# Optimization experiments

Measured on AMD Instinct MI355X. Metric: run time of the kernel, lower is better.

The kernel has to match this reference:

```python
import jax, jax.numpy as jnp
import numpy as np

NUM_GROUPS = 32
EPS = 1e-5


def group_norm(x, scale, bias):
    # x: [b, c, h, w]
    b, c, h, w = x.shape
    xg = x.reshape(b, NUM_GROUPS, c // NUM_GROUPS, h, w)
    mean = jnp.mean(xg, axis=(2, 3, 4), keepdims=True)
    var = jnp.var(xg, axis=(2, 3, 4), keepdims=True)
    xg = (xg - mean) * jax.lax.rsqrt(var + EPS)
    xn = xg.reshape(b, c, h, w)
    return xn * scale[None, :, None, None] + bias[None, :, None, None]


def conv1x1(x, w, b):
    # x: [b, c_in, h, w], w: [c_out, c_in], b: [c_out]
    return jnp.einsum('bchw,dc->bdhw', x, w) + b[None, :, None, None]


def setup_inputs() -> dict:
    key = jax.random.key(0)
    ks = jax.random.split(key, 11)
    B, C, H, W = 16, 512, 32, 32
    s = 1.0 / np.sqrt(C)
    inp = {
        'x': jax.random.normal(ks[0], (B, C, H, W), jnp.float32),
        'gn_scale': jnp.ones((C,), jnp.float32),
        'gn_bias': jnp.zeros((C,), jnp.float32),
        'wq': jax.random.normal(ks[1], (C, C), jnp.float32) * s,
        'bq': jnp.zeros((C,), jnp.float32),
        'wk': jax.random.normal(ks[2], (C, C), jnp.float32) * s,
        'bk': jnp.zeros((C,), jnp.float32),
        'wv': jax.random.normal(ks[3], (C, C), jnp.float32) * s,
        'bv': jnp.zeros((C,), jnp.float32),
        'wp': jax.random.normal(ks[4], (C, C), jnp.float32) * s,
        'bp': jnp.zeros((C,), jnp.float32),
    }
    return inp


def reference(x, gn_scale, gn_bias, wq, bq, wk, bk, wv, bv, wp, bp):
    b, c, h, w = x.shape
    xn = group_norm(x, gn_scale, gn_bias)
    q = conv1x1(xn, wq, bq).reshape(b, c, h * w)  # [b, c, n]
    k = conv1x1(xn, wk, bk).reshape(b, c, h * w)
    v = conv1x1(xn, wv, bv).reshape(b, c, h * w)
    # attn[b, i, j] = sum_c q[b, c, i] * k[b, c, j]
    attn = jnp.einsum('bci,bcj->bij', q, k) * (c ** -0.5)
    A = jax.nn.softmax(attn, axis=-1)
    # out[b, c, i] = sum_j A[b, i, j] * v[b, c, j]
    out = jnp.einsum('bij,bcj->bci', A, v).reshape(b, c, h, w)
    scores = conv1x1(out, wp, bp)
    return x + scores
```

## Files before the change

kernel.cpp:

```cpp
#include <hip/hip_runtime.h>

typedef __bf16 bf16x8 __attribute__((ext_vector_type(8)));
typedef float  f32x4  __attribute__((ext_vector_type(4)));

__device__ __forceinline__ unsigned short f2bf(float f) {
    union { float f; unsigned int u; } x; x.f = f;
    unsigned int r = (x.u + 0x7FFFu + ((x.u >> 16) & 1u)) >> 16;
    return (unsigned short)r;
}

typedef const __attribute__((address_space(1))) unsigned short gu16;
typedef __attribute__((address_space(3)))       unsigned short lu16;
__device__ __forceinline__ void gl_lds16(const unsigned short* g, unsigned short* l) {
    __builtin_amdgcn_global_load_lds((gu16*)g, (lu16*)l, 16, 0, 0);
}

__device__ __forceinline__ void stage8(
    const unsigned short* __restrict__ Ab, int lda,
    const unsigned short* __restrict__ Bb, int ldb,
    unsigned short* LB, int s, int s_max, int wave, int lane)
{
    if (s >= s_max) return;
    const int tau  = s >> 2;
    const int pi   = s & 3;
    const int isA  = pi >> 1;
    const int half = pi & 1;
    unsigned short* dst = LB + (isA ? 0 : 32768) + (tau & 1) * 16384 + half * 8192 + wave * 512;
    const unsigned short* src = isA ? Ab : Bb;
    const int ld = isA ? lda : ldb;
    const int R  = half * 128 + wave * 8 + (lane >> 3);
    const int kc = tau * 64 + (((lane & 7) ^ ((lane >> 5) << 1)) << 3);
    gl_lds16(src + (long)R * ld + kc,        dst);
    gl_lds16(src + (long)(R + 64) * ld + kc, dst + 4096);
}

template<int NT>
__device__ __forceinline__ void gemm8_core(
    const unsigned short* __restrict__ Ab, int lda,
    const unsigned short* __restrict__ Bb, int ldb,
    f32x4 (&acc)[8][4], unsigned short* LB)
{
    const int tid  = threadIdx.x;
    const int lane = tid & 63;
    const int wave = tid >> 6;
    const int wM   = wave >> 2;
    const int wN   = wave & 3;
    const int l16  = lane & 15;
    const int quad = lane >> 4;
    const int ckx  = quad ^ (((l16 >> 2) & 1) << 1);
    const int aoff = wM * 8192 + l16 * 64 + ckx * 8;
    const int boff = 32768 + (wN >> 1) * 8192 + ((wN & 1) * 64 + l16) * 64 + ckx * 8;

    #pragma unroll
    for (int s = 0; s < 7; ++s)
        stage8(Ab, lda, Bb, ldb, LB, s, 4 * NT, wave, lane);
    asm volatile("s_waitcnt vmcnt(6)" ::: "memory");
    __builtin_amdgcn_s_barrier();
    __builtin_amdgcn_sched_barrier(0);

    bf16x8 af[4][2], bf[4][2];

#define RD_A(buf, mh)                                                         \
    _Pragma("unroll")                                                         \
    for (int m = 0; m < 4; ++m)                                               \
        _Pragma("unroll")                                                     \
        for (int kk = 0; kk < 2; ++kk)                                        \
            af[m][kk] = *(const bf16x8*)&LB[(buf) * 16384 + aoff + ((mh) * 4 + m) * 1024 + kk * 32];
#define RD_B(buf)                                                             \
    _Pragma("unroll")                                                         \
    for (int n = 0; n < 4; ++n)                                               \
        _Pragma("unroll")                                                     \
        for (int kk = 0; kk < 2; ++kk)                                        \
            bf[n][kk] = *(const bf16x8*)&LB[(buf) * 16384 + boff + n * 1024 + kk * 32];
#define MF(mh, nh)                                                            \
    __builtin_amdgcn_s_setprio(1);                                            \
    _Pragma("unroll")                                                         \
    for (int m = 0; m < 4; ++m)                                               \
        _Pragma("unroll")                                                     \
        for (int n = 0; n < 2; ++n)                                           \
            _Pragma("unroll")                                                 \
            for (int kk = 0; kk < 2; ++kk)                                    \
                acc[(mh)*4+m][(nh)*2+n] = __builtin_amdgcn_mfma_f32_16x16x32_bf16( \
                    af[m][kk], bf[(nh)*2+n][kk], acc[(mh)*4+m][(nh)*2+n], 0, 0, 0); \
    __builtin_amdgcn_s_setprio(0);
#define BARS do { __builtin_amdgcn_s_barrier(); __builtin_amdgcn_sched_barrier(0); } while (0)
#define LGW  do { asm volatile("s_waitcnt lgkmcnt(0)" ::: "memory"); __builtin_amdgcn_sched_barrier(0); } while (0)

    const int NITER = NT / 2;
    for (int i = 0; i < NITER; ++i) {
        const int s0 = 6 + 8 * i;
        RD_B(0) RD_A(0, 0)
        stage8(Ab, lda, Bb, ldb, LB, s0 + 1, 4 * NT, wave, lane);
        BARS; LGW;
        MF(0, 0)
        BARS;
        stage8(Ab, lda, Bb, ldb, LB, s0 + 2, 4 * NT, wave, lane);
        BARS;
        MF(0, 1)
        BARS;
        RD_A(0, 1)
        stage8(Ab, lda, Bb, ldb, LB, s0 + 3, 4 * NT, wave, lane);
        BARS; LGW;
        MF(1, 0)
        BARS;
        stage8(Ab, lda, Bb, ldb, LB, s0 + 4, 4 * NT, wave, lane);
        BARS;
        MF(1, 1)
        if (i == NITER - 1) { asm volatile("s_waitcnt vmcnt(0)" ::: "memory"); }
        else                { asm volatile("s_waitcnt vmcnt(6)" ::: "memory"); }
        BARS;
        RD_B(1) RD_A(1, 0)
        stage8(Ab, lda, Bb, ldb, LB, s0 + 5, 4 * NT, wave, lane);
        BARS; LGW;
        MF(0, 0)
        BARS;
        stage8(Ab, lda, Bb, ldb, LB, s0 + 6, 4 * NT, wave, lane);
        BARS;
        MF(0, 1)
        BARS;
        RD_A(1, 1)
        stage8(Ab, lda, Bb, ldb, LB, s0 + 7, 4 * NT, wave, lane);
        BARS; LGW;
        MF(1, 0)
        BARS;
        stage8(Ab, lda, Bb, ldb, LB, s0 + 8, 4 * NT, wave, lane);
        BARS;
        MF(1, 1)
        if (i < NITER - 1) { asm volatile("s_waitcnt vmcnt(6)" ::: "memory"); }
        BARS;
    }
#undef RD_A
#undef RD_B
#undef MF
#undef BARS
#undef LGW
}

__global__ __launch_bounds__(512, 2) void p8_k(
    const unsigned short* __restrict__ qT,
    const unsigned short* __restrict__ kT,
    unsigned short* __restrict__ Sb,
    float* __restrict__ lsum,
    float alpha)
{
    __shared__ __align__(16) unsigned short LB[65536];
    const int z = blockIdx.z;
    const unsigned short* Ab = qT + (long)z * 524288 + (long)(blockIdx.y * 256) * 512;
    const unsigned short* Bb = kT + (long)z * 524288 + (long)(blockIdx.x * 256) * 512;
    f32x4 acc[8][4] = {};
    gemm8_core<8>(Ab, 512, Bb, 512, acc, LB);

    const int lane = threadIdx.x & 63, wave = threadIdx.x >> 6;
    const int wM = wave >> 2, wN = wave & 3;
    const int l16 = lane & 15, quad = lane >> 4;
    const int gm0 = blockIdx.y * 256 + wM * 128;
    const int gn0 = blockIdx.x * 256 + wN * 64;
    unsigned short* scr = LB + wave * 8192;

    float rs[8][4];
    #pragma unroll
    for (int mi = 0; mi < 8; ++mi) { rs[mi][0] = rs[mi][1] = rs[mi][2] = rs[mi][3] = 0.f; }
    #pragma unroll
    for (int mi = 0; mi < 8; ++mi)
        #pragma unroll
        for (int ni = 0; ni < 4; ++ni) {
            f32x4 v = acc[mi][ni];
            #pragma unroll
            for (int r = 0; r < 4; ++r) {
                float e = __expf(v[r] * alpha);
                rs[mi][r] += e;
                const int row = mi * 16 + quad * 4 + r;
                const int col = ni * 16 + l16;
                scr[row * 64 + (((col >> 3) ^ (row & 7)) << 3) + (col & 7)] = f2bf(e);
            }
        }
    #pragma unroll
    for (int mi = 0; mi < 8; ++mi)
        #pragma unroll
        for (int r = 0; r < 4; ++r) {
            float s = rs[mi][r];
            s += __shfl_xor(s, 1); s += __shfl_xor(s, 2);
            s += __shfl_xor(s, 4); s += __shfl_xor(s, 8);
            if (l16 == 0)
                atomicAdd(&lsum[(long)z * 1024 + gm0 + mi * 16 + quad * 4 + r], s);
        }
    unsigned short* dst = Sb + (long)z * 1048576;
    #pragma unroll
    for (int it = 0; it < 16; ++it) {
        const int row = it * 8 + (lane >> 3);
        const int ck  = lane & 7;
        uint4 vv = *(uint4*)&scr[row * 64 + ((ck ^ (row & 7)) << 3)];
        *(uint4*)&dst[(long)(gm0 + row) * 1024 + gn0 + ck * 8] = vv;
    }
}

__global__ __launch_bounds__(512, 2) void qkv8_k(
    const unsigned short* __restrict__ Wqkv,
    const unsigned short* __restrict__ xnT,
    unsigned short* __restrict__ qT,
    unsigned short* __restrict__ kT,
    unsigned short* __restrict__ vB,
    const float* __restrict__ bqkv)
{
    __shared__ __align__(16) unsigned short LB[65536];
    const int z = blockIdx.z;
    const unsigned short* Ab = Wqkv + (long)(blockIdx.y * 256) * 512;
    const unsigned short* Bb = xnT + (long)z * 524288 + (long)(blockIdx.x * 256) * 512;
    f32x4 acc[8][4] = {};
    gemm8_core<8>(Ab, 512, Bb, 512, acc, LB);

    const int lane = threadIdx.x & 63, wave = threadIdx.x >> 6;
    const int wM = wave >> 2, wN = wave & 3;
    const int l16 = lane & 15, quad = lane >> 4;
    const int gm0 = blockIdx.y * 256 + wM * 128;
    const int gn0 = blockIdx.x * 256 + wN * 64;
    const int mat = blockIdx.y >> 1;
    const int ml0 = gm0 & 511;
    const long zb = (long)z * 524288;
    unsigned short* scr = LB + wave * 8192;

    if (mat == 2) {
        #pragma unroll
        for (int mi = 0; mi < 8; ++mi)
            #pragma unroll
            for (int ni = 0; ni < 4; ++ni) {
                f32x4 v = acc[mi][ni];
                #pragma unroll
                for (int r = 0; r < 4; ++r) {
                    const int row = mi * 16 + quad * 4 + r;
                    const int col = ni * 16 + l16;
                    scr[row * 64 + (((col >> 3) ^ (row & 7)) << 3) + (col & 7)] =
                        f2bf(v[r] + bqkv[gm0 + row]);
                }
            }
        #pragma unroll
        for (int it = 0; it < 16; ++it) {
            const int row = it * 8 + (lane >> 3);
            const int ck  = lane & 7;
            uint4 vv = *(uint4*)&scr[row * 64 + ((ck ^ (row & 7)) << 3)];
            *(uint4*)&vB[zb + (long)(ml0 + row) * 1024 + gn0 + ck * 8] = vv;
        }
    } else {
        unsigned short* dstm = (mat == 0) ? qT : kT;
        #pragma unroll
        for (int mi = 0; mi < 8; ++mi)
            #pragma unroll
            for (int ni = 0; ni < 4; ++ni) {
                f32x4 v = acc[mi][ni];
                const int nl = ni * 16 + l16;
                const int ch = mi * 2 + (quad >> 1);
                const int m4 = gm0 + mi * 16 + quad * 4;
                ushort4 p;
                p.x = f2bf(v[0] + bqkv[m4 + 0]);
                p.y = f2bf(v[1] + bqkv[m4 + 1]);
                p.z = f2bf(v[2] + bqkv[m4 + 2]);
                p.w = f2bf(v[3] + bqkv[m4 + 3]);
                *(ushort4*)&scr[nl * 128 + ((ch ^ (nl & 15)) << 3) + (quad & 1) * 4] = p;
            }
        #pragma unroll
        for (int it = 0; it < 16; ++it) {
            const int nl  = it * 4 + (lane >> 4);
            const int chl = lane & 15;
            uint4 vv = *(uint4*)&scr[nl * 128 + ((chl ^ (nl & 15)) << 3)];
            *(uint4*)&dstm[zb + (long)(gn0 + nl) * 512 + ml0 + chl * 8] = vv;
        }
    }
}

__device__ __forceinline__ void stage_tiles(
    const unsigned short* __restrict__ Ab, int lda,
    const unsigned short* __restrict__ Bb, int ldb,
    int k0, unsigned short* Ad, unsigned short* Bd,
    int wave, int r0, int c0)
{
    gl_lds16(Ab + (long)r0 * lda + c0 + k0,        Ad + wave * 512);
    gl_lds16(Ab + (long)(r0 + 64) * lda + c0 + k0, Ad + 2048 + wave * 512);
    gl_lds16(Bb + (long)r0 * ldb + c0 + k0,        Bd + wave * 512);
    gl_lds16(Bb + (long)(r0 + 64) * ldb + c0 + k0, Bd + 2048 + wave * 512);
}

__device__ __forceinline__ void gemm_core_db(
    const unsigned short* __restrict__ Ab, int lda,
    const unsigned short* __restrict__ Bb, int ldb,
    int K, f32x4 (&acc)[4][4],
    unsigned short* As, unsigned short* Bs)
{
    const int tid  = threadIdx.x;
    const int lane = tid & 63;
    const int wave = tid >> 6;
    const int wm   = (wave >> 1) * 64;
    const int wn   = (wave & 1) * 64;
    const int l16  = lane & 15;
    const int quad = lane >> 4;

    const int r0 = wave * 16 + (lane >> 2);
    const int c0 = ((lane & 3) ^ ((lane >> 3) & 3)) * 8;

    stage_tiles(Ab, lda, Bb, ldb, 0, As, Bs, wave, r0, c0);

    const int sw8 = ((l16 >> 1) & 3) * 8;

    int sel = 0;
    for (int k0 = 0; k0 < K; k0 += 32) {
        __syncthreads();
        if (k0 + 32 < K)
            stage_tiles(Ab, lda, Bb, ldb, k0 + 32,
                        As + (sel ^ 1) * 4096, Bs + (sel ^ 1) * 4096, wave, r0, c0);

        const unsigned short* Ap = As + sel * 4096;
        const unsigned short* Bp = Bs + sel * 4096;
        bf16x8 af[4], bfr[4];
        #pragma unroll
        for (int mi = 0; mi < 4; mi++)
            af[mi] = *(const bf16x8*)&Ap[(wm + mi * 16 + l16) * 32 + ((quad * 8) ^ sw8)];
        #pragma unroll
        for (int ni = 0; ni < 4; ni++)
            bfr[ni] = *(const bf16x8*)&Bp[(wn + ni * 16 + l16) * 32 + ((quad * 8) ^ sw8)];
        #pragma unroll
        for (int mi = 0; mi < 4; mi++)
            #pragma unroll
            for (int ni = 0; ni < 4; ni++)
                acc[mi][ni] = __builtin_amdgcn_mfma_f32_16x16x32_bf16(af[mi], bfr[ni], acc[mi][ni], 0, 0, 0);
        sel ^= 1;
    }
}

template<typename OutT, bool TRANS_OUT, bool HAS_BIAS, bool HAS_RESID,
         bool EXP_SUM, bool ROW_SCALE>
__global__ __launch_bounds__(256) void gemm_k(
    const unsigned short* __restrict__ Ag, long sA, int lda,
    const unsigned short* __restrict__ Bg, long sB, int ldb,
    OutT* __restrict__ Cg, long sC, int ldc,
    const float* __restrict__ bias,
    const float* __restrict__ resid, long sR,
    float* __restrict__ lsum, long sL,
    float alpha, int K)
{
    __shared__ __align__(16) unsigned short LB[16384];
    unsigned short* As = LB;
    unsigned short* Bs = LB + 8192;

    const unsigned short* Ab = Ag + (long)blockIdx.z * sA + (long)(blockIdx.y * 128) * lda;
    const unsigned short* Bb = Bg + (long)blockIdx.z * sB + (long)(blockIdx.x * 128) * ldb;

    f32x4 acc[4][4] = {};
    gemm_core_db(Ab, lda, Bb, ldb, K, acc, As, Bs);

    const int lane = threadIdx.x & 63;
    const int wave = threadIdx.x >> 6;
    const int l16  = lane & 15;
    const int quad = lane >> 4;
    const int mb = blockIdx.y * 128 + (wave >> 1) * 64;
    const int nb = blockIdx.x * 128 + (wave & 1) * 64;

    if constexpr (sizeof(OutT) == 2) {
        __syncthreads();
        unsigned short* scr = LB + wave * 4096;

        #pragma unroll
        for (int mi = 0; mi < 4; mi++) {
            float rsum[4];
            if constexpr (EXP_SUM) { rsum[0] = rsum[1] = rsum[2] = rsum[3] = 0.f; }
            #pragma unroll
            for (int ni = 0; ni < 4; ni++) {
                f32x4 v = acc[mi][ni];
                float invl;
                if constexpr (ROW_SCALE) invl = 1.f / lsum[(long)blockIdx.z * sL + nb + ni * 16 + l16];
                float o[4];
                #pragma unroll
                for (int r = 0; r < 4; r++) {
                    float val = v[r] * alpha;
                    if constexpr (HAS_BIAS) val += bias[mb + mi * 16 + quad * 4 + r];
                    if constexpr (EXP_SUM) { val = __expf(val); rsum[r] += val; }
                    if constexpr (ROW_SCALE) val *= invl;
                    o[r] = val;
                }
                if constexpr (TRANS_OUT) {
                    const int nl = ni * 16 + l16;
                    const int ch = mi * 2 + (quad >> 1);
                    ushort4 p; p.x = f2bf(o[0]); p.y = f2bf(o[1]); p.z = f2bf(o[2]); p.w = f2bf(o[3]);
                    *(ushort4*)&scr[nl * 64 + ((ch ^ (nl & 7)) * 8) + (quad & 1) * 4] = p;
                } else {
                    #pragma unroll
                    for (int r = 0; r < 4; r++) {
                        const int ml = mi * 16 + quad * 4 + r;
                        const int nc = ni * 2 + (l16 >> 3);
                        scr[ml * 64 + ((nc ^ (ml & 7)) * 8) + (l16 & 7)] = f2bf(o[r]);
                    }
                }
            }
            if constexpr (EXP_SUM) {
                const int m0 = mb + mi * 16 + quad * 4;
                #pragma unroll
                for (int r = 0; r < 4; r++) {
                    float s = rsum[r];
                    s += __shfl_xor(s, 1); s += __shfl_xor(s, 2);
                    s += __shfl_xor(s, 4); s += __shfl_xor(s, 8);
                    if (l16 == 0)
                        atomicAdd(&lsum[(long)blockIdx.z * sL + m0 + r], s);
                }
            }
        }
        __syncthreads();

        const int ch2 = lane & 7;
        const int rr  = lane >> 3;
        unsigned short* Cs = (unsigned short*)Cg + (long)blockIdx.z * sC;
        if constexpr (TRANS_OUT) {
            unsigned short* dst = Cs + mb + ch2 * 8;
            #pragma unroll
            for (int it = 0; it < 8; it++) {
                const int nl = rr + it * 8;
                uint4 v = *(uint4*)&scr[nl * 64 + ((ch2 ^ (nl & 7)) * 8)];
                *(uint4*)(dst + (long)(nb + nl) * ldc) = v;
            }
        } else {
            unsigned short* dst = Cs + nb + ch2 * 8;
            #pragma unroll
            for (int it = 0; it < 8; it++) {
                const int ml = rr + it * 8;
                uint4 v = *(uint4*)&scr[ml * 64 + ((ch2 ^ (ml & 7)) * 8)];
                *(uint4*)(dst + (long)(mb + ml) * ldc) = v;
            }
        }
    } else {
        #pragma unroll
        for (int mi = 0; mi < 4; mi++) {
            #pragma unroll
            for (int ni = 0; ni < 4; ni++) {
                f32x4 v = acc[mi][ni];
                const int m0 = mb + mi * 16 + quad * 4;
                const int n  = nb + ni * 16 + l16;
                const long base = (long)blockIdx.z * sC;
                #pragma unroll
                for (int r = 0; r < 4; r++) {
                    float val = v[r] * alpha;
                    if (HAS_BIAS) val += bias[m0 + r];
                    if (HAS_RESID) val += resid[(long)blockIdx.z * sR + (long)(m0 + r) * ldc + n];
                    ((float*)Cg)[base + (long)(m0 + r) * ldc + n] = val;
                }
            }
        }
    }
}

__global__ __launch_bounds__(256) void gn_k(
    const float* __restrict__ x, const float* __restrict__ gsc,
    const float* __restrict__ gbi, unsigned short* __restrict__ xnT)
{
    __shared__ __align__(16) unsigned short ln[16 * 1024];
    __shared__ float red[8];
    const int b = blockIdx.y, g = blockIdx.x;
    const int tid = threadIdx.x, lane = tid & 63, wv = tid >> 6;

    const float4* x4 = (const float4*)(x + ((long)b * 512 + g * 16) * 1024);
    float4 vals[16];
    float s = 0.f, ss = 0.f;
    #pragma unroll
    for (int i = 0; i < 16; i++) {
        float4 v = x4[tid + i * 256];
        vals[i] = v;
        s  += v.x + v.y + v.z + v.w;
        ss += v.x * v.x + v.y * v.y + v.z * v.z + v.w * v.w;
    }
    for (int o = 32; o; o >>= 1) { s += __shfl_down(s, o); ss += __shfl_down(ss, o); }
    if (lane == 0) { red[wv * 2] = s; red[wv * 2 + 1] = ss; }
    __syncthreads();
    const float S  = red[0] + red[2] + red[4] + red[6];
    const float SS = red[1] + red[3] + red[5] + red[7];
    const float mean = S * (1.f / 16384.f);
    const float var  = SS * (1.f / 16384.f) - mean * mean;
    const float inv  = rsqrtf(var + 1e-5f);

    #pragma unroll
    for (int i = 0; i < 16; i++) {
        const int idx = tid + i * 256;
        const int c   = idx >> 8;
        const float sc = gsc[g * 16 + c] * inv;
        const float bi = gbi[g * 16 + c] - mean * sc;
        float4 v = vals[i];
        ushort4 p;
        p.x = f2bf(v.x * sc + bi); p.y = f2bf(v.y * sc + bi);
        p.z = f2bf(v.z * sc + bi); p.w = f2bf(v.w * sc + bi);
        ((ushort4*)ln)[idx] = p;
    }
    __syncthreads();

    unsigned short* op = xnT + (long)b * 1024 * 512 + g * 16;
    for (int rep = 0; rep < 4; rep++) {
        const int n = rep * 256 + tid;
        union { unsigned short u[16]; uint4 v[2]; } t;
        #pragma unroll
        for (int c = 0; c < 16; c++) t.u[c] = ln[c * 1024 + n];
        *(uint4*)&op[(long)n * 512]     = t.v[0];
        *(uint4*)&op[(long)n * 512 + 8] = t.v[1];
    }
}

__global__ __launch_bounds__(256) void wconv_k(
    const float* __restrict__ w0, const float* __restrict__ w1,
    const float* __restrict__ w2, const float* __restrict__ w3,
    const float* __restrict__ b0, const float* __restrict__ b1,
    const float* __restrict__ b2,
    unsigned short* __restrict__ out, float* __restrict__ bqkv,
    float* __restrict__ lsum)
{
    const int m = blockIdx.y;
    const int i = blockIdx.x * 256 + threadIdx.x;
    if (m == 4) {
        if (i < 384) {
            const int which = i >> 7, off = i & 127;
            const float* src = (which == 0) ? b0 : (which == 1) ? b1 : b2;
            ((float4*)bqkv)[i] = ((const float4*)src)[off];
        }
        if (i < 16384) lsum[i] = 0.f;
        return;
    }
    const float* src = (m == 0) ? w0 : (m == 1) ? w1 : (m == 2) ? w2 : w3;
    float4 v = ((const float4*)src)[i];
    ushort4 o; o.x = f2bf(v.x); o.y = f2bf(v.y); o.z = f2bf(v.z); o.w = f2bf(v.w);
    ((ushort4*)(out + (long)m * 262144))[i] = o;
}

extern "C" void kernel_launch(void* const* d_in, const int* in_sizes, int n_in,
                              void* d_out, int out_size, void* d_ws, size_t ws_size,
                              hipStream_t stream)
{
    const float* x   = (const float*)d_in[0];
    const float* gsc = (const float*)d_in[1];
    const float* gbi = (const float*)d_in[2];
    const float* wq  = (const float*)d_in[3];
    const float* bq  = (const float*)d_in[4];
    const float* wk  = (const float*)d_in[5];
    const float* bk  = (const float*)d_in[6];
    const float* wv  = (const float*)d_in[7];
    const float* bv  = (const float*)d_in[8];
    const float* wp  = (const float*)d_in[9];
    const float* bp  = (const float*)d_in[10];
    float* out = (float*)d_out;

    char* ws = (char*)d_ws;
    unsigned short* xnT = (unsigned short*)(ws);
    unsigned short* qT  = (unsigned short*)(ws + 16777216);
    unsigned short* kT  = (unsigned short*)(ws + 33554432);
    unsigned short* vB  = (unsigned short*)(ws + 50331648);
    unsigned short* Sb  = (unsigned short*)(ws + 67108864);
    unsigned short* Wb  = (unsigned short*)(ws + 100663296);
    float*          bqkv= (float*)        (ws + 102760448);
    float*          Lb  = (float*)        (ws + 102768640);
    unsigned short* OT  = xnT;

    const long sBCN = 512L * 1024;

    wconv_k<<<dim3(256, 5), 256, 0, stream>>>(wq, wk, wv, wp, bq, bk, bv, Wb, bqkv, Lb);
    gn_k<<<dim3(32, 16), 256, 0, stream>>>(x, gsc, gbi, xnT);

    qkv8_k<<<dim3(4, 6, 16), 512, 0, stream>>>(Wb, xnT, qT, kT, vB, bqkv);

    p8_k<<<dim3(4, 4, 16), 512, 0, stream>>>(qT, kT, Sb, Lb, 0.044194173824159216f);

    gemm_k<unsigned short, true, false, false, false, true>
        <<<dim3(8, 4, 16), 256, 0, stream>>>(
        vB, sBCN, 1024, Sb, 1048576L, 1024, OT, sBCN, 512,
        nullptr, nullptr, 0, Lb, 1024, 1.f, 1024);

    gemm_k<float, false, true, true, false, false>
        <<<dim3(8, 4, 16), 256, 0, stream>>>(
        Wb + 786432, 0, 512, OT, sBCN, 512, out, sBCN, 1024, bp, x, sBCN,
        nullptr, 0, 1.f, 512);
}
```

Before: 224.4 us.

## Generalize 8-wave pipelined GEMM core to 128-row tiles; use for QKV and AV

Templates the 8-wave global_load_lds pipelined GEMM core on the A-tile height so it can run with 128-row A tiles. The QKV projection moves to 128x256 tiles with twice as many blocks, and the attention-times-V GEMM moves from the 4-wave double-buffered kernel to this deeper pipeline. Weight conversion is merged into the group-norm launch to save one launch, and the generic gemm_k is specialised into a final projection kernel. The aim is better load balance across CUs and more latency hiding in the AV GEMM, with less B-tile reuse per block as the trade-off.

```diff
diff --git a/kernel.cpp b/kernel.cpp
--- a/kernel.cpp
+++ b/kernel.cpp
@@ -15,30 +15,35 @@
     __builtin_amdgcn_global_load_lds((gu16*)g, (lu16*)l, 16, 0, 0);
 }
 
-__device__ __forceinline__ void stage8(
+template<int NT, int BMH>
+__device__ __forceinline__ void stage8g(
     const unsigned short* __restrict__ Ab, int lda,
     const unsigned short* __restrict__ Bb, int ldb,
-    unsigned short* LB, int s, int s_max, int wave, int lane)
-{
-    if (s >= s_max) return;
+    unsigned short* LB, int s, int wave, int lane)
+{
+    if (s >= 4 * NT) return;
     const int tau  = s >> 2;
     const int pi   = s & 3;
-    const int isA  = pi >> 1;
     const int half = pi & 1;
-    unsigned short* dst = LB + (isA ? 0 : 32768) + (tau & 1) * 16384 + half * 8192 + wave * 512;
-    const unsigned short* src = isA ? Ab : Bb;
-    const int ld = isA ? lda : ldb;
-    const int R  = half * 128 + wave * 8 + (lane >> 3);
-    const int kc = tau * 64 + (((lane & 7) ^ ((lane >> 5) << 1)) << 3);
-    gl_lds16(src + (long)R * ld + kc,        dst);
-    gl_lds16(src + (long)(R + 64) * ld + kc, dst + 4096);
-}
-
-template<int NT>
+    const int kc   = tau * 64 + (((lane & 7) ^ ((lane >> 5) << 1)) << 3);
+    if (pi >= 2) {
+        unsigned short* dst = LB + (tau & 1) * (BMH * 8192) + half * (BMH * 4096) + wave * 512;
+        const int R = half * (BMH * 64) + wave * 8 + (lane >> 3);
+        gl_lds16(Ab + (long)R * lda + kc, dst);
+        if constexpr (BMH == 2) gl_lds16(Ab + (long)(R + 64) * lda + kc, dst + 4096);
+    } else {
+        unsigned short* dst = LB + (BMH * 16384) + (tau & 1) * 16384 + half * 8192 + wave * 512;
+        const int R = half * 128 + wave * 8 + (lane >> 3);
+        gl_lds16(Bb + (long)R * ldb + kc, dst);
+        gl_lds16(Bb + (long)(R + 64) * ldb + kc, dst + 4096);
+    }
+}
+
+template<int NT, int BMH>
 __device__ __forceinline__ void gemm8_core(
     const unsigned short* __restrict__ Ab, int lda,
     const unsigned short* __restrict__ Bb, int ldb,
-    f32x4 (&acc)[8][4], unsigned short* LB)
+    f32x4 (&acc)[4 * BMH][4], unsigned short* LB)
 {
     const int tid  = threadIdx.x;
     const int lane = tid & 63;
@@ -48,24 +53,27 @@
     const int l16  = lane & 15;
     const int quad = lane >> 4;
     const int ckx  = quad ^ (((l16 >> 2) & 1) << 1);
-    const int aoff = wM * 8192 + l16 * 64 + ckx * 8;
-    const int boff = 32768 + (wN >> 1) * 8192 + ((wN & 1) * 64 + l16) * 64 + ckx * 8;
+    const int aoff = wM * (BMH * 4096) + l16 * 64 + ckx * 8;
+    const int boff = BMH * 16384 + (wN >> 1) * 8192 + ((wN & 1) * 64 + l16) * 64 + ckx * 8;
+
+#define VMW do { if constexpr (BMH == 2) asm volatile("s_waitcnt vmcnt(6)" ::: "memory"); \
+                 else                    asm volatile("s_waitcnt vmcnt(5)" ::: "memory"); } while (0)
 
     #pragma unroll
     for (int s = 0; s < 7; ++s)
-        stage8(Ab, lda, Bb, ldb, LB, s, 4 * NT, wave, lane);
-    asm volatile("s_waitcnt vmcnt(6)" ::: "memory");
+        stage8g<NT, BMH>(Ab, lda, Bb, ldb, LB, s, wave, lane);
+    VMW;
     __builtin_amdgcn_s_barrier();
     __builtin_amdgcn_sched_barrier(0);
 
-    bf16x8 af[4][2], bf[4][2];
+    bf16x8 af[2 * BMH][2], bf[4][2];
 
 #define RD_A(buf, mh)                                                         \
     _Pragma("unroll")                                                         \
-    for (int m = 0; m < 4; ++m)                                               \
+    for (int m = 0; m < 2 * BMH; ++m)                                         \
         _Pragma("unroll")                                                     \
         for (int kk = 0; kk < 2; ++kk)                                        \
-            af[m][kk] = *(const bf16x8*)&LB[(buf) * 16384 + aoff + ((mh) * 4 + m) * 1024 + kk * 32];
+            af[m][kk] = *(const bf16x8*)&LB[(buf) * (BMH * 8192) + aoff + ((mh) * 2 * BMH + m) * 1024 + kk * 32];
 #define RD_B(buf)                                                             \
     _Pragma("unroll")                                                         \
     for (int n = 0; n < 4; ++n)                                               \
@@ -75,13 +83,13 @@
 #define MF(mh, nh)                                                            \
     __builtin_amdgcn_s_setprio(1);                                            \
     _Pragma("unroll")                                                         \
-    for (int m = 0; m < 4; ++m)                                               \
+    for (int m = 0; m < 2 * BMH; ++m)                                         \
         _Pragma("unroll")                                                     \
         for (int n = 0; n < 2; ++n)                                           \
             _Pragma("unroll")                                                 \
             for (int kk = 0; kk < 2; ++kk)                                    \
-                acc[(mh)*4+m][(nh)*2+n] = __builtin_amdgcn_mfma_f32_16x16x32_bf16( \
-                    af[m][kk], bf[(nh)*2+n][kk], acc[(mh)*4+m][(nh)*2+n], 0, 0, 0); \
+                acc[(mh) * 2 * BMH + m][(nh) * 2 + n] = __builtin_amdgcn_mfma_f32_16x16x32_bf16( \
+                    af[m][kk], bf[(nh) * 2 + n][kk], acc[(mh) * 2 * BMH + m][(nh) * 2 + n], 0, 0, 0); \
     __builtin_amdgcn_s_setprio(0);
 #define BARS do { __builtin_amdgcn_s_barrier(); __builtin_amdgcn_sched_barrier(0); } while (0)
 #define LGW  do { asm volatile("s_waitcnt lgkmcnt(0)" ::: "memory"); __builtin_amdgcn_sched_barrier(0); } while (0)
@@ -90,43 +98,43 @@
     for (int i = 0; i < NITER; ++i) {
         const int s0 = 6 + 8 * i;
         RD_B(0) RD_A(0, 0)
-        stage8(Ab, lda, Bb, ldb, LB, s0 + 1, 4 * NT, wave, lane);
+        stage8g<NT, BMH>(Ab, lda, Bb, ldb, LB, s0 + 1, wave, lane);
         BARS; LGW;
         MF(0, 0)
         BARS;
-        stage8(Ab, lda, Bb, ldb, LB, s0 + 2, 4 * NT, wave, lane);
+        stage8g<NT, BMH>(Ab, lda, Bb, ldb, LB, s0 + 2, wave, lane);
         BARS;
         MF(0, 1)
         BARS;
         RD_A(0, 1)
-        stage8(Ab, lda, Bb, ldb, LB, s0 + 3, 4 * NT, wave, lane);
+        stage8g<NT, BMH>(Ab, lda, Bb, ldb, LB, s0 + 3, wave, lane);
         BARS; LGW;
         MF(1, 0)
         BARS;
-        stage8(Ab, lda, Bb, ldb, LB, s0 + 4, 4 * NT, wave, lane);
+        stage8g<NT, BMH>(Ab, lda, Bb, ldb, LB, s0 + 4, wave, lane);
         BARS;
         MF(1, 1)
         if (i == NITER - 1) { asm volatile("s_waitcnt vmcnt(0)" ::: "memory"); }
-        else                { asm volatile("s_waitcnt vmcnt(6)" ::: "memory"); }
+        else                { VMW; }
         BARS;
         RD_B(1) RD_A(1, 0)
-        stage8(Ab, lda, Bb, ldb, LB, s0 + 5, 4 * NT, wave, lane);
+        stage8g<NT, BMH>(Ab, lda, Bb, ldb, LB, s0 + 5, wave, lane);
         BARS; LGW;
         MF(0, 0)
         BARS;
-        stage8(Ab, lda, Bb, ldb, LB, s0 + 6, 4 * NT, wave, lane);
+        stage8g<NT, BMH>(Ab, lda, Bb, ldb, LB, s0 + 6, wave, lane);
         BARS;
         MF(0, 1)
         BARS;
         RD_A(1, 1)
-        stage8(Ab, lda, Bb, ldb, LB, s0 + 7, 4 * NT, wave, lane);
+        stage8g<NT, BMH>(Ab, lda, Bb, ldb, LB, s0 + 7, wave, lane);
         BARS; LGW;
         MF(1, 0)
         BARS;
-        stage8(Ab, lda, Bb, ldb, LB, s0 + 8, 4 * NT, wave, lane);
+        stage8g<NT, BMH>(Ab, lda, Bb, ldb, LB, s0 + 8, wave, lane);
         BARS;
         MF(1, 1)
-        if (i < NITER - 1) { asm volatile("s_waitcnt vmcnt(6)" ::: "memory"); }
+        if (i < NITER - 1) { VMW; }
         BARS;
     }
 #undef RD_A
@@ -134,6 +142,7 @@
 #undef MF
 #undef BARS
 #undef LGW
+#undef VMW
 }
 
 __global__ __launch_bounds__(512, 2) void p8_k(
@@ -148,7 +157,7 @@
     const unsigned short* Ab = qT + (long)z * 524288 + (long)(blockIdx.y * 256) * 512;
     const unsigned short* Bb = kT + (long)z * 524288 + (long)(blockIdx.x * 256) * 512;
     f32x4 acc[8][4] = {};
-    gemm8_core<8>(Ab, 512, Bb, 512, acc, LB);
+    gemm8_core<8, 2>(Ab, 512, Bb, 512, acc, LB);
 
     const int lane = threadIdx.x & 63, wave = threadIdx.x >> 6;
     const int wM = wave >> 2, wN = wave & 3;
@@ -202,48 +211,48 @@
     unsigned short* __restrict__ vB,
     const float* __restrict__ bqkv)
 {
-    __shared__ __align__(16) unsigned short LB[65536];
+    __shared__ __align__(16) unsigned short LB[49152];
     const int z = blockIdx.z;
-    const unsigned short* Ab = Wqkv + (long)(blockIdx.y * 256) * 512;
+    const unsigned short* Ab = Wqkv + (long)(blockIdx.y * 128) * 512;
     const unsigned short* Bb = xnT + (long)z * 524288 + (long)(blockIdx.x * 256) * 512;
-    f32x4 acc[8][4] = {};
-    gemm8_core<8>(Ab, 512, Bb, 512, acc, LB);
+    f32x4 acc[4][4] = {};
+    gemm8_core<8, 1>(Ab, 512, Bb, 512, acc, LB);
 
     const int lane = threadIdx.x & 63, wave = threadIdx.x >> 6;
     const int wM = wave >> 2, wN = wave & 3;
     const int l16 = lane & 15, quad = lane >> 4;
-    const int gm0 = blockIdx.y * 256 + wM * 128;
+    const int gm0 = blockIdx.y * 128 + wM * 64;
     const int gn0 = blockIdx.x * 256 + wN * 64;
-    const int mat = blockIdx.y >> 1;
+    const int mat = blockIdx.y >> 2;
     const int ml0 = gm0 & 511;
     const long zb = (long)z * 524288;
-    unsigned short* scr = LB + wave * 8192;
+    unsigned short* scr = LB + wave * 4096;
 
     if (mat == 2) {
         #pragma unroll
-        for (int mi = 0; mi < 8; ++mi)
+        for (int mi = 0; mi < 4; ++mi)
             #pragma unroll
             for (int ni = 0; ni < 4; ++ni) {
                 f32x4 v = acc[mi][ni];
                 #pragma unroll
                 for (int r = 0; r < 4; ++r) {
-                    const int row = mi * 16 + quad * 4 + r;
-                    const int col = ni * 16 + l16;
-                    scr[row * 64 + (((col >> 3) ^ (row & 7)) << 3) + (col & 7)] =
-                        f2bf(v[r] + bqkv[gm0 + row]);
+                    const int ml = mi * 16 + quad * 4 + r;
+                    const int nc = ni * 2 + (l16 >> 3);
+                    scr[ml * 64 + ((nc ^ (ml & 7)) * 8) + (l16 & 7)] = f2bf(v[r] + bqkv[gm0 + ml]);
                 }
             }
-        #pragma unroll
-        for (int it = 0; it < 16; ++it) {
-            const int row = it * 8 + (lane >> 3);
-            const int ck  = lane & 7;
-            uint4 vv = *(uint4*)&scr[row * 64 + ((ck ^ (row & 7)) << 3)];
-            *(uint4*)&vB[zb + (long)(ml0 + row) * 1024 + gn0 + ck * 8] = vv;
+        const int ch2 = lane & 7, rr = lane >> 3;
+        unsigned short* dst = vB + zb + gn0 + ch2 * 8;
+        #pragma unroll
+        for (int it = 0; it < 8; ++it) {
+            const int ml = rr + it * 8;
+            uint4 vv = *(uint4*)&scr[ml * 64 + ((ch2 ^ (ml & 7)) * 8)];
+            *(uint4*)(dst + (long)(ml0 + ml) * 1024) = vv;
         }
     } else {
         unsigned short* dstm = (mat == 0) ? qT : kT;
         #pragma unroll
-        for (int mi = 0; mi < 8; ++mi)
+        for (int mi = 0; mi < 4; ++mi)
             #pragma unroll
             for (int ni = 0; ni < 4; ++ni) {
                 f32x4 v = acc[mi][ni];
@@ -255,15 +264,59 @@
                 p.y = f2bf(v[1] + bqkv[m4 + 1]);
                 p.z = f2bf(v[2] + bqkv[m4 + 2]);
                 p.w = f2bf(v[3] + bqkv[m4 + 3]);
-                *(ushort4*)&scr[nl * 128 + ((ch ^ (nl & 15)) << 3) + (quad & 1) * 4] = p;
+                *(ushort4*)&scr[nl * 64 + ((ch ^ (nl & 7)) * 8) + (quad & 1) * 4] = p;
             }
-        #pragma unroll
-        for (int it = 0; it < 16; ++it) {
-            const int nl  = it * 4 + (lane >> 4);
-            const int chl = lane & 15;
-            uint4 vv = *(uint4*)&scr[nl * 128 + ((chl ^ (nl & 15)) << 3)];
-            *(uint4*)&dstm[zb + (long)(gn0 + nl) * 512 + ml0 + chl * 8] = vv;
-        }
+        const int ch2 = lane & 7, rr = lane >> 3;
+        unsigned short* dst = dstm + zb + ml0 + ch2 * 8;
+        #pragma unroll
+        for (int it = 0; it < 8; ++it) {
+            const int nl = rr + it * 8;
+            uint4 vv = *(uint4*)&scr[nl * 64 + ((ch2 ^ (nl & 7)) * 8)];
+            *(uint4*)(dst + (long)(gn0 + nl) * 512) = vv;
+        }
+    }
+}
+
+__global__ __launch_bounds__(512, 2) void av8_k(
+    const unsigned short* __restrict__ vB,
+    const unsigned short* __restrict__ Sb,
+    unsigned short* __restrict__ OT,
+    const float* __restrict__ Lb)
+{
+    __shared__ __align__(16) unsigned short LB[49152];
+    const int z = blockIdx.z;
+    const unsigned short* Ab = vB + (long)z * 524288 + (long)(blockIdx.y * 128) * 1024;
+    const unsigned short* Bb = Sb + (long)z * 1048576 + (long)(blockIdx.x * 256) * 1024;
+    f32x4 acc[4][4] = {};
+    gemm8_core<16, 1>(Ab, 1024, Bb, 1024, acc, LB);
+
+    const int lane = threadIdx.x & 63, wave = threadIdx.x >> 6;
+    const int wM = wave >> 2, wN = wave & 3;
+    const int l16 = lane & 15, quad = lane >> 4;
+    const int gm0 = blockIdx.y * 128 + wM * 64;
+    const int gn0 = blockIdx.x * 256 + wN * 64;
+    unsigned short* scr = LB + wave * 4096;
+
+    #pragma unroll
+    for (int mi = 0; mi < 4; ++mi)
+        #pragma unroll
+        for (int ni = 0; ni < 4; ++ni) {
+            f32x4 v = acc[mi][ni];
+            const float invl = 1.f / Lb[(long)z * 1024 + gn0 + ni * 16 + l16];
+            const int nl = ni * 16 + l16;
+            const int ch = mi * 2 + (quad >> 1);
+            ushort4 p;
+            p.x = f2bf(v[0] * invl); p.y = f2bf(v[1] * invl);
+            p.z = f2bf(v[2] * invl); p.w = f2bf(v[3] * invl);
+            *(ushort4*)&scr[nl * 64 + ((ch ^ (nl & 7)) * 8) + (quad & 1) * 4] = p;
+        }
+    const int ch2 = lane & 7, rr = lane >> 3;
+    unsigned short* dst = OT + (long)z * 524288 + gm0 + ch2 * 8;
+    #pragma unroll
+    for (int it = 0; it < 8; ++it) {
+        const int nl = rr + it * 8;
+        uint4 vv = *(uint4*)&scr[nl * 64 + ((ch2 ^ (nl & 7)) * 8)];
+        *(uint4*)(dst + (long)(gn0 + nl) * 512) = vv;
     }
 }
 
@@ -325,26 +378,22 @@
     }
 }
 
-template<typename OutT, bool TRANS_OUT, bool HAS_BIAS, bool HAS_RESID,
-         bool EXP_SUM, bool ROW_SCALE>
-__global__ __launch_bounds__(256) void gemm_k(
-    const unsigned short* __restrict__ Ag, long sA, int lda,
-    const unsigned short* __restrict__ Bg, long sB, int ldb,
-    OutT* __restrict__ Cg, long sC, int ldc,
+__global__ __launch_bounds__(256) void fin_k(
+    const unsigned short* __restrict__ Wp,
+    const unsigned short* __restrict__ OTb,
+    float* __restrict__ out,
     const float* __restrict__ bias,
-    const float* __restrict__ resid, long sR,
-    float* __restrict__ lsum, long sL,
-    float alpha, int K)
+    const float* __restrict__ resid)
 {
     __shared__ __align__(16) unsigned short LB[16384];
     unsigned short* As = LB;
     unsigned short* Bs = LB + 8192;
 
-    const unsigned short* Ab = Ag + (long)blockIdx.z * sA + (long)(blockIdx.y * 128) * lda;
-    const unsigned short* Bb = Bg + (long)blockIdx.z * sB + (long)(blockIdx.x * 128) * ldb;
+    const unsigned short* Ab = Wp + (long)(blockIdx.y * 128) * 512;
+    const unsigned short* Bb = OTb + (long)blockIdx.z * 524288 + (long)(blockIdx.x * 128) * 512;
 
     f32x4 acc[4][4] = {};
-    gemm_core_db(Ab, lda, Bb, ldb, K, acc, As, Bs);
+    gemm_core_db(Ab, 512, Bb, 512, 512, acc, As, Bs);
 
     const int lane = threadIdx.x & 63;
     const int wave = threadIdx.x >> 6;
@@ -353,105 +402,60 @@
     const int mb = blockIdx.y * 128 + (wave >> 1) * 64;
     const int nb = blockIdx.x * 128 + (wave & 1) * 64;
 
-    if constexpr (sizeof(OutT) == 2) {
-        __syncthreads();
-        unsigned short* scr = LB + wave * 4096;
-
-        #pragma unroll
-        for (int mi = 0; mi < 4; mi++) {
-            float rsum[4];
-            if constexpr (EXP_SUM) { rsum[0] = rsum[1] = rsum[2] = rsum[3] = 0.f; }
+    #pragma unroll
+    for (int mi = 0; mi < 4; mi++) {
+        #pragma unroll
+        for (int ni = 0; ni < 4; ni++) {
+            f32x4 v = acc[mi][ni];
+            const int m0 = mb + mi * 16 + quad * 4;
+            const int n  = nb + ni * 16 + l16;
+            const long base = (long)blockIdx.z * 524288;
             #pragma unroll
-            for (int ni = 0; ni < 4; ni++) {
-                f32x4 v = acc[mi][ni];
-                float invl;
-                if constexpr (ROW_SCALE) invl = 1.f / lsum[(long)blockIdx.z * sL + nb + ni * 16 + l16];
-                float o[4];
-                #pragma unroll
-                for (int r = 0; r < 4; r++) {
-                    float val = v[r] * alpha;
-                    if constexpr (HAS_BIAS) val += bias[mb + mi * 16 + quad * 4 + r];
-                    if constexpr (EXP_SUM) { val = __expf(val); rsum[r] += val; }
-                    if constexpr (ROW_SCALE) val *= invl;
-                    o[r] = val;
-                }
-                if constexpr (TRANS_OUT) {
-                    const int nl = ni * 16 + l16;
-                    const int ch = mi * 2 + (quad >> 1);
-                    ushort4 p; p.x = f2bf(o[0]); p.y = f2bf(o[1]); p.z = f2bf(o[2]); p.w = f2bf(o[3]);
-                    *(ushort4*)&scr[nl * 64 + ((ch ^ (nl & 7)) * 8) + (quad & 1) * 4] = p;
-                } else {
-                    #pragma unroll
-                    for (int r = 0; r < 4; r++) {
-                        const int ml = mi * 16 + quad * 4 + r;
-                        const int nc = ni * 2 + (l16 >> 3);
-                        scr[ml * 64 + ((nc ^ (ml & 7)) * 8) + (l16 & 7)] = f2bf(o[r]);
-                    }
-                }
+            for (int r = 0; r < 4; r++) {
+                float val = v[r] + bias[m0 + r] + resid[base + (long)(m0 + r) * 1024 + n];
+                out[base + (long)(m0 + r) * 1024 + n] = val;
             }
-            if constexpr (EXP_SUM) {
-                const int m0 = mb + mi * 16 + quad * 4;
-                #pragma unroll
-                for (int r = 0; r < 4; r++) {
-                    float s = rsum[r];
-                    s += __shfl_xor(s, 1); s += __shfl_xor(s, 2);
-                    s += __shfl_xor(s, 4); s += __shfl_xor(s, 8);
-                    if (l16 == 0)
-                        atomicAdd(&lsum[(long)blockIdx.z * sL + m0 + r], s);
-                }
-            }
-        }
-        __syncthreads();
-
-        const int ch2 = lane & 7;
-        const int rr  = lane >> 3;
-        unsigned short* Cs = (unsigned short*)Cg + (long)blockIdx.z * sC;
-        if constexpr (TRANS_OUT) {
-            unsigned short* dst = Cs + mb + ch2 * 8;
-            #pragma unroll
-            for (int it = 0; it < 8; it++) {
-                const int nl = rr + it * 8;
-                uint4 v = *(uint4*)&scr[nl * 64 + ((ch2 ^ (nl & 7)) * 8)];
-                *(uint4*)(dst + (long)(nb + nl) * ldc) = v;
-            }
-        } else {
-            unsigned short* dst = Cs + nb + ch2 * 8;
-            #pragma unroll
-            for (int it = 0; it < 8; it++) {
-                const int ml = rr + it * 8;
-                uint4 v = *(uint4*)&scr[ml * 64 + ((ch2 ^ (ml & 7)) * 8)];
-                *(uint4*)(dst + (long)(mb + ml) * ldc) = v;
-            }
-        }
-    } else {
-        #pragma unroll
-        for (int mi = 0; mi < 4; mi++) {
-            #pragma unroll
-            for (int ni = 0; ni < 4; ni++) {
-                f32x4 v = acc[mi][ni];
-                const int m0 = mb + mi * 16 + quad * 4;
-                const int n  = nb + ni * 16 + l16;
-                const long base = (long)blockIdx.z * sC;
-                #pragma unroll
-                for (int r = 0; r < 4; r++) {
-                    float val = v[r] * alpha;
-                    if (HAS_BIAS) val += bias[m0 + r];
-                    if (HAS_RESID) val += resid[(long)blockIdx.z * sR + (long)(m0 + r) * ldc + n];
-                    ((float*)Cg)[base + (long)(m0 + r) * ldc + n] = val;
-                }
-            }
-        }
-    }
-}
-
-__global__ __launch_bounds__(256) void gn_k(
+        }
+    }
+}
+
+__global__ __launch_bounds__(256) void gnw_k(
     const float* __restrict__ x, const float* __restrict__ gsc,
-    const float* __restrict__ gbi, unsigned short* __restrict__ xnT)
+    const float* __restrict__ gbi, unsigned short* __restrict__ xnT,
+    const float* __restrict__ w0, const float* __restrict__ w1,
+    const float* __restrict__ w2, const float* __restrict__ w3,
+    const float* __restrict__ b0, const float* __restrict__ b1,
+    const float* __restrict__ b2,
+    unsigned short* __restrict__ wout, float* __restrict__ bqkv,
+    float* __restrict__ lsum)
 {
     __shared__ __align__(16) unsigned short ln[16 * 1024];
     __shared__ float red[8];
-    const int b = blockIdx.y, g = blockIdx.x;
-    const int tid = threadIdx.x, lane = tid & 63, wv = tid >> 6;
+    const int bid = blockIdx.x;
+    const int tid = threadIdx.x;
+
+    if (bid >= 512) {
+        const int j = bid - 512;
+        const int m = j >> 8;
+        const int i = (j & 255) * 256 + tid;
+        if (m == 4) {
+            if (i < 384) {
+                const int which = i >> 7, off = i & 127;
+                const float* src = (which == 0) ? b0 : (which == 1) ? b1 : b2;
+                ((float4*)bqkv)[i] = ((const float4*)src)[off];
+            }
+            if (i < 16384) lsum[i] = 0.f;
+            return;
+        }
+        const float* src = (m == 0) ? w0 : (m == 1) ? w1 : (m == 2) ? w2 : w3;
+        float4 v = ((const float4*)src)[i];
+        ushort4 o; o.x = f2bf(v.x); o.y = f2bf(v.y); o.z = f2bf(v.z); o.w = f2bf(v.w);
+        ((ushort4*)(wout + (long)m * 262144))[i] = o;
+        return;
+    }
+
+    const int b = bid >> 5, g = bid & 31;
+    const int lane = tid & 63, wv = tid >> 6;
 
     const float4* x4 = (const float4*)(x + ((long)b * 512 + g * 16) * 1024);
     float4 vals[16];
@@ -495,31 +499,6 @@
         *(uint4*)&op[(long)n * 512]     = t.v[0];
         *(uint4*)&op[(long)n * 512 + 8] = t.v[1];
     }
-}
-
-__global__ __launch_bounds__(256) void wconv_k(
-    const float* __restrict__ w0, const float* __restrict__ w1,
-    const float* __restrict__ w2, const float* __restrict__ w3,
-    const float* __restrict__ b0, const float* __restrict__ b1,
-    const float* __restrict__ b2,
-    unsigned short* __restrict__ out, float* __restrict__ bqkv,
-    float* __restrict__ lsum)
-{
-    const int m = blockIdx.y;
-    const int i = blockIdx.x * 256 + threadIdx.x;
-    if (m == 4) {
-        if (i < 384) {
-            const int which = i >> 7, off = i & 127;
-            const float* src = (which == 0) ? b0 : (which == 1) ? b1 : b2;
-            ((float4*)bqkv)[i] = ((const float4*)src)[off];
-        }
-        if (i < 16384) lsum[i] = 0.f;
-        return;
-    }
-    const float* src = (m == 0) ? w0 : (m == 1) ? w1 : (m == 2) ? w2 : w3;
-    float4 v = ((const float4*)src)[i];
-    ushort4 o; o.x = f2bf(v.x); o.y = f2bf(v.y); o.z = f2bf(v.z); o.w = f2bf(v.w);
-    ((ushort4*)(out + (long)m * 262144))[i] = o;
 }
 
 extern "C" void kernel_launch(void* const* d_in, const int* in_sizes, int n_in,
@@ -550,22 +529,14 @@
     float*          Lb  = (float*)        (ws + 102768640);
     unsigned short* OT  = xnT;
 
-    const long sBCN = 512L * 1024;
-
-    wconv_k<<<dim3(256, 5), 256, 0, stream>>>(wq, wk, wv, wp, bq, bk, bv, Wb, bqkv, Lb);
-    gn_k<<<dim3(32, 16), 256, 0, stream>>>(x, gsc, gbi, xnT);
-
-    qkv8_k<<<dim3(4, 6, 16), 512, 0, stream>>>(Wb, xnT, qT, kT, vB, bqkv);
+    gnw_k<<<1792, 256, 0, stream>>>(x, gsc, gbi, xnT,
+                                    wq, wk, wv, wp, bq, bk, bv, Wb, bqkv, Lb);
+
+    qkv8_k<<<dim3(4, 12, 16), 512, 0, stream>>>(Wb, xnT, qT, kT, vB, bqkv);
 
     p8_k<<<dim3(4, 4, 16), 512, 0, stream>>>(qT, kT, Sb, Lb, 0.044194173824159216f);
 
-    gemm_k<unsigned short, true, false, false, false, true>
-        <<<dim3(8, 4, 16), 256, 0, stream>>>(
-        vB, sBCN, 1024, Sb, 1048576L, 1024, OT, sBCN, 512,
-        nullptr, nullptr, 0, Lb, 1024, 1.f, 1024);
-
-    gemm_k<float, false, true, true, false, false>
-        <<<dim3(8, 4, 16), 256, 0, stream>>>(
-        Wb + 786432, 0, 512, OT, sBCN, 512, out, sBCN, 1024, bp, x, sBCN,
-        nullptr, 0, 1.f, 512);
-}
+    av8_k<<<dim3(4, 4, 16), 512, 0, stream>>>(vB, Sb, OT, Lb);
+
+    fin_k<<<dim3(8, 4, 16), 256, 0, stream>>>(Wb + 786432, OT, out, bp, x);
+}
```

After: 219.4 us. 1.02x faster.
